# Optimization experiments

Measured on AMD Instinct MI355X. Metric: run time of the kernel, lower is better.

## Reference

```python
import jax, jax.numpy as jnp
import numpy as np

B, S, D = 4, 512, 512


def setup_inputs() -> dict:
    key = jax.random.key(0)
    k0, k1, k2 = jax.random.split(key, 3)
    x = jax.random.normal(k0, (B, S, D), jnp.float32)
    W1 = jax.random.normal(k1, (D, D // 2), jnp.float32) / np.sqrt(D).astype(np.float32)
    b1 = jnp.zeros((D // 2,), jnp.float32)
    W2 = jax.random.normal(k2, (D // 2, 1), jnp.float32) / np.sqrt(D // 2).astype(np.float32)
    b2 = jnp.zeros((1,), jnp.float32)
    # deterministic ragged durations in the module's ~10-30 frame range
    durations = jnp.broadcast_to(8 + (jnp.arange(S, dtype=jnp.int32) % 32), (B, S))
    total_length = int(np.asarray(durations).sum())  # 48128, static
    return dict(x=x, W1=W1, b1=b1, W2=W2, b2=b2, durations=durations,
                total_length=total_length)


def reference(x, W1, b1, W2, b2, durations, total_length):
    # --- duration-predictor MLP (Linear -> ReLU -> Linear -> Softplus) ---
    h = jax.nn.relu(jnp.einsum('bsd,df->bsf', x, W1) + b1)
    dur_mlp = jax.nn.softplus(jnp.einsum('bsf,fo->bso', h, W2) + b2)[..., 0]  # [B,S]

    # --- length regulation: gather + linear interpolation ---
    # torch code uses durations of batch row 0 for all batch elements, and
    # allocates total_length = sum over the WHOLE batch (trailing zeros kept).
    dur0 = durations[0].astype(jnp.int32)          # [S]
    csum = jnp.cumsum(dur0)                         # [S], csum[-1] = used length L
    L = csum[-1]
    t = jnp.arange(total_length, dtype=jnp.int32)   # [T]
    tok = jnp.searchsorted(csum, t, side='right')   # token index per output frame
    valid = t < L
    ic = jnp.minimum(tok, S - 1)
    j = t - (csum[ic] - dur0[ic])                   # offset within token's frames
    # last token: pure repeat (alpha=0); others: lerp toward x[:, i+1]
    alpha = jnp.where(ic == S - 1, 0.0,
                      j.astype(x.dtype) / dur0[ic].astype(x.dtype))  # [T]
    left = x[:, ic]                                 # [B,T,D]
    right = x[:, jnp.minimum(ic + 1, S - 1)]        # [B,T,D]
    a = alpha[None, :, None]
    expanded = (1.0 - a) * left + a * right
    expanded = jnp.where(valid[None, :, None], expanded, 0.0)
    return expanded, dur_mlp
```

## Files before the change

### kernel.cpp

```cpp
#include <hip/hip_runtime.h>
#include <math.h>

#define Bn 4
#define Sn 512
#define Dn 512
#define Fn 256
#define RROWS 8

struct Ent { float alpha; int ic; };

typedef float v4f __attribute__((ext_vector_type(4)));

__global__ __launch_bounds__(512) void prep_kernel(const int* __restrict__ dur,
                                                   Ent* __restrict__ tab, int T) {
    __shared__ int csum[Sn];
    int tid = threadIdx.x;
    csum[tid] = dur[tid];
    __syncthreads();
    #pragma unroll
    for (int off = 1; off < Sn; off <<= 1) {
        int add = (tid >= off) ? csum[tid - off] : 0;
        __syncthreads();
        csum[tid] += add;
        __syncthreads();
    }
    int L = csum[Sn - 1];
    int t = blockIdx.x * Sn + tid;
    if (t >= T) return;
    Ent e;
    if (t >= L) {
        e.alpha = 0.f; e.ic = -1;
    } else {
        int lo = 0, hi = Sn;
        while (lo < hi) {
            int mid = (lo + hi) >> 1;
            if (csum[mid] <= t) lo = mid + 1; else hi = mid;
        }
        int ic = lo;
        int start = ic ? csum[ic - 1] : 0;
        int d = csum[ic] - start;
        e.ic = ic;
        e.alpha = (ic == Sn - 1) ? 0.f : (float)(t - start) / (float)d;
    }
    tab[t] = e;
}

__global__ __launch_bounds__(256) void mlp_kernel(const float* __restrict__ x,
                                                  const float* __restrict__ W1,
                                                  const float* __restrict__ b1,
                                                  const float* __restrict__ W2,
                                                  const float* __restrict__ b2,
                                                  float* __restrict__ out_dur) {
    __shared__ float xs[RROWS][Dn];
    __shared__ float red[4][RROWS];
    int f = threadIdx.x;
    int r0 = blockIdx.x * RROWS;

    const float4* src = (const float4*)(x + (size_t)r0 * Dn);
    float4* dst = (float4*)(&xs[0][0]);
    for (int i = f; i < RROWS * Dn / 4; i += 256) dst[i] = src[i];
    __syncthreads();

    float acc[RROWS];
    #pragma unroll
    for (int r = 0; r < RROWS; r++) acc[r] = 0.f;

    for (int k = 0; k < Dn; k += 4) {
        float w0 = W1[(k + 0) * Fn + f];
        float w1 = W1[(k + 1) * Fn + f];
        float w2 = W1[(k + 2) * Fn + f];
        float w3 = W1[(k + 3) * Fn + f];
        #pragma unroll
        for (int r = 0; r < RROWS; r++) {
            float4 xv = *(const float4*)&xs[r][k];
            acc[r] += xv.x * w0 + xv.y * w1 + xv.z * w2 + xv.w * w3;
        }
    }

    float bb = b1[f], wf = W2[f];
    float p[RROWS];
    #pragma unroll
    for (int r = 0; r < RROWS; r++) {
        float h = acc[r] + bb;
        h = h > 0.f ? h : 0.f;
        p[r] = h * wf;
    }

    int lane = f & 63, wv = f >> 6;
    #pragma unroll
    for (int r = 0; r < RROWS; r++) {
        float v = p[r];
        #pragma unroll
        for (int off = 32; off > 0; off >>= 1) v += __shfl_down(v, off, 64);
        if (lane == 0) red[wv][r] = v;
    }
    __syncthreads();
    if (f < RROWS) {
        float z = red[0][f] + red[1][f] + red[2][f] + red[3][f] + b2[0];
        float sp = fmaxf(z, 0.f) + log1pf(expf(-fabsf(z)));
        out_dur[r0 + f] = sp;
    }
}

__global__ __launch_bounds__(256) void expand_kernel(const float* __restrict__ x,
                                                     const Ent* __restrict__ tab,
                                                     float* __restrict__ out, int T) {
    int idx = blockIdx.x * 256 + threadIdx.x;
    int total = T << 7;
    if (idx >= total) return;
    int b = blockIdx.y;
    int t = idx >> 7;
    int d4 = idx & 127;

    Ent e = tab[t];
    float4 res;
    if (e.ic < 0) {
        res = make_float4(0.f, 0.f, 0.f, 0.f);
    } else {
        const float* xb = x + (size_t)b * (Sn * Dn);
        int icr = e.ic + 1; if (icr > Sn - 1) icr = Sn - 1;
        float4 l = ((const float4*)(xb + (size_t)e.ic * Dn))[d4];
        float4 r = ((const float4*)(xb + (size_t)icr * Dn))[d4];
        float a = e.alpha, na = 1.f - a;
        res.x = na * l.x + a * r.x;
        res.y = na * l.y + a * r.y;
        res.z = na * l.z + a * r.z;
        res.w = na * l.w + a * r.w;
    }
    float4* op = (float4*)(out + ((size_t)b * T + t) * Dn) + d4;
    __builtin_nontemporal_store(*(const v4f*)&res, (v4f*)op);
}

extern "C" void kernel_launch(void* const* d_in, const int* in_sizes, int n_in,
                              void* d_out, int out_size, void* d_ws, size_t ws_size,
                              hipStream_t stream) {
    const float* x   = (const float*)d_in[0];
    const float* W1  = (const float*)d_in[1];
    const float* b1  = (const float*)d_in[2];
    const float* W2  = (const float*)d_in[3];
    const float* b2  = (const float*)d_in[4];
    const int* durs  = (const int*)d_in[5];
    float* out = (float*)d_out;

    int T = (out_size - Bn * Sn) / (Bn * Dn);
    Ent* tab = (Ent*)d_ws;

    dim3 pgrid((T + Sn - 1) / Sn);
    prep_kernel<<<pgrid, Sn, 0, stream>>>(durs, tab, T);

    float* dur_out = out + ((size_t)out_size - Bn * Sn);
    mlp_kernel<<<dim3((Bn * Sn) / RROWS), 256, 0, stream>>>(x, W1, b1, W2, b2, dur_out);

    int total4 = T * (Dn / 4);
    dim3 egrid((total4 + 255) / 256, Bn);
    expand_kernel<<<egrid, 256, 0, stream>>>(x, tab, out, T);
}
```

Baseline: 427.6 us.

## Merge prep and MLP kernels into one launch; give expand one wavefront per frame

```diff
diff --git a/kernel.cpp b/kernel.cpp
--- a/kernel.cpp
+++ b/kernel.cpp
@@ -11,124 +11,126 @@
 
 typedef float v4f __attribute__((ext_vector_type(4)));
 
-__global__ __launch_bounds__(512) void prep_kernel(const int* __restrict__ dur,
-                                                   Ent* __restrict__ tab, int T) {
-    __shared__ int csum[Sn];
+#define PREP_BLKS (48128 / 256)
+#define MLP_BLKS  ((Bn * Sn) / RROWS)
+
+__global__ __launch_bounds__(256) void prep_mlp_kernel(
+        const int* __restrict__ dur, Ent* __restrict__ tab, int T,
+        const float* __restrict__ x,  const float* __restrict__ W1,
+        const float* __restrict__ b1, const float* __restrict__ W2,
+        const float* __restrict__ b2, float* __restrict__ out_dur) {
     int tid = threadIdx.x;
-    csum[tid] = dur[tid];
-    __syncthreads();
-    #pragma unroll
-    for (int off = 1; off < Sn; off <<= 1) {
-        int add = (tid >= off) ? csum[tid - off] : 0;
+
+    if (blockIdx.x < PREP_BLKS) {
+        __shared__ int cs[Sn];
+        cs[tid]       = dur[tid];
+        cs[tid + 256] = dur[tid + 256];
         __syncthreads();
-        csum[tid] += add;
+        #pragma unroll
+        for (int off = 1; off < Sn; off <<= 1) {
+            int a0 = (tid >= off) ? cs[tid - off] : 0;
+            int p1 = tid + 256;
+            int a1 = (p1 >= off) ? cs[p1 - off] : 0;
+            __syncthreads();
+            cs[tid] += a0; cs[p1] += a1;
+            __syncthreads();
+        }
+        int L = cs[Sn - 1];
+        int t = blockIdx.x * 256 + tid;
+        if (t >= T) return;
+        Ent e;
+        if (t >= L) {
+            e.alpha = 0.f; e.ic = -1;
+        } else {
+            int lo = 0, hi = Sn;
+            while (lo < hi) {
+                int mid = (lo + hi) >> 1;
+                if (cs[mid] <= t) lo = mid + 1; else hi = mid;
+            }
+            int ic = lo;
+            int start = ic ? cs[ic - 1] : 0;
+            int d = cs[ic] - start;
+            e.ic = ic;
+            e.alpha = (ic == Sn - 1) ? 0.f : (float)(t - start) / (float)d;
+        }
+        tab[t] = e;
+    } else {
+        __shared__ float xs[RROWS][Dn];
+        __shared__ float red[4][RROWS];
+        int f = tid;
+        int r0 = (blockIdx.x - PREP_BLKS) * RROWS;
+
+        const float4* src = (const float4*)(x + (size_t)r0 * Dn);
+        float4* dst = (float4*)(&xs[0][0]);
+        for (int i = f; i < RROWS * Dn / 4; i += 256) dst[i] = src[i];
         __syncthreads();
-    }
-    int L = csum[Sn - 1];
-    int t = blockIdx.x * Sn + tid;
-    if (t >= T) return;
-    Ent e;
-    if (t >= L) {
-        e.alpha = 0.f; e.ic = -1;
-    } else {
-        int lo = 0, hi = Sn;
-        while (lo < hi) {
-            int mid = (lo + hi) >> 1;
-            if (csum[mid] <= t) lo = mid + 1; else hi = mid;
+
+        float acc[RROWS];
+        #pragma unroll
+        for (int r = 0; r < RROWS; r++) acc[r] = 0.f;
+
+        for (int k = 0; k < Dn; k += 4) {
+            float w0 = W1[(k + 0) * Fn + f];
+            float w1 = W1[(k + 1) * Fn + f];
+            float w2 = W1[(k + 2) * Fn + f];
+            float w3 = W1[(k + 3) * Fn + f];
+            #pragma unroll
+            for (int r = 0; r < RROWS; r++) {
+                float4 xv = *(const float4*)&xs[r][k];
+                acc[r] += xv.x * w0 + xv.y * w1 + xv.z * w2 + xv.w * w3;
+            }
         }
-        int ic = lo;
-        int start = ic ? csum[ic - 1] : 0;
-        int d = csum[ic] - start;
-        e.ic = ic;
-        e.alpha = (ic == Sn - 1) ? 0.f : (float)(t - start) / (float)d;
-    }
-    tab[t] = e;
-}
 
-__global__ __launch_bounds__(256) void mlp_kernel(const float* __restrict__ x,
-                                                  const float* __restrict__ W1,
-                                                  const float* __restrict__ b1,
-                                                  const float* __restrict__ W2,
-                                                  const float* __restrict__ b2,
-                                                  float* __restrict__ out_dur) {
-    __shared__ float xs[RROWS][Dn];
-    __shared__ float red[4][RROWS];
-    int f = threadIdx.x;
-    int r0 = blockIdx.x * RROWS;
-
-    const float4* src = (const float4*)(x + (size_t)r0 * Dn);
-    float4* dst = (float4*)(&xs[0][0]);
-    for (int i = f; i < RROWS * Dn / 4; i += 256) dst[i] = src[i];
-    __syncthreads();
-
-    float acc[RROWS];
-    #pragma unroll
-    for (int r = 0; r < RROWS; r++) acc[r] = 0.f;
-
-    for (int k = 0; k < Dn; k += 4) {
-        float w0 = W1[(k + 0) * Fn + f];
-        float w1 = W1[(k + 1) * Fn + f];
-        float w2 = W1[(k + 2) * Fn + f];
-        float w3 = W1[(k + 3) * Fn + f];
+        float bb = b1[f], wf = W2[f];
+        int lane = f & 63, wv = f >> 6;
         #pragma unroll
         for (int r = 0; r < RROWS; r++) {
-            float4 xv = *(const float4*)&xs[r][k];
-            acc[r] += xv.x * w0 + xv.y * w1 + xv.z * w2 + xv.w * w3;
+            float h = acc[r] + bb;
+            h = h > 0.f ? h : 0.f;
+            float v = h * wf;
+            #pragma unroll
+            for (int off = 32; off > 0; off >>= 1) v += __shfl_down(v, off, 64);
+            if (lane == 0) red[wv][r] = v;
         }
-    }
-
-    float bb = b1[f], wf = W2[f];
-    float p[RROWS];
-    #pragma unroll
-    for (int r = 0; r < RROWS; r++) {
-        float h = acc[r] + bb;
-        h = h > 0.f ? h : 0.f;
-        p[r] = h * wf;
-    }
-
-    int lane = f & 63, wv = f >> 6;
-    #pragma unroll
-    for (int r = 0; r < RROWS; r++) {
-        float v = p[r];
-        #pragma unroll
-        for (int off = 32; off > 0; off >>= 1) v += __shfl_down(v, off, 64);
-        if (lane == 0) red[wv][r] = v;
-    }
-    __syncthreads();
-    if (f < RROWS) {
-        float z = red[0][f] + red[1][f] + red[2][f] + red[3][f] + b2[0];
-        float sp = fmaxf(z, 0.f) + log1pf(expf(-fabsf(z)));
-        out_dur[r0 + f] = sp;
+        __syncthreads();
+        if (f < RROWS) {
+            float z = red[0][f] + red[1][f] + red[2][f] + red[3][f] + b2[0];
+            float sp = fmaxf(z, 0.f) + log1pf(expf(-fabsf(z)));
+            out_dur[r0 + f] = sp;
+        }
     }
 }
 
 __global__ __launch_bounds__(256) void expand_kernel(const float* __restrict__ x,
                                                      const Ent* __restrict__ tab,
                                                      float* __restrict__ out, int T) {
-    int idx = blockIdx.x * 256 + threadIdx.x;
-    int total = T << 7;
-    if (idx >= total) return;
+    int lane = threadIdx.x & 63;
+    int r = threadIdx.x >> 6;
+    int t = blockIdx.x * 4 + r;
     int b = blockIdx.y;
-    int t = idx >> 7;
-    int d4 = idx & 127;
 
     Ent e = tab[t];
-    float4 res;
+    float* orow = out + ((size_t)b * T + t) * Dn;
+
     if (e.ic < 0) {
-        res = make_float4(0.f, 0.f, 0.f, 0.f);
+        v4f z = {0.f, 0.f, 0.f, 0.f};
+        __builtin_nontemporal_store(z, (v4f*)orow + lane);
+        __builtin_nontemporal_store(z, (v4f*)orow + lane + 64);
     } else {
         const float* xb = x + (size_t)b * (Sn * Dn);
         int icr = e.ic + 1; if (icr > Sn - 1) icr = Sn - 1;
-        float4 l = ((const float4*)(xb + (size_t)e.ic * Dn))[d4];
-        float4 r = ((const float4*)(xb + (size_t)icr * Dn))[d4];
+        const float4* lp = (const float4*)(xb + (size_t)e.ic * Dn);
+        const float4* rp = (const float4*)(xb + (size_t)icr * Dn);
         float a = e.alpha, na = 1.f - a;
-        res.x = na * l.x + a * r.x;
-        res.y = na * l.y + a * r.y;
-        res.z = na * l.z + a * r.z;
-        res.w = na * l.w + a * r.w;
+        float4 l0 = lp[lane],      r0 = rp[lane];
+        float4 l1 = lp[lane + 64], r1 = rp[lane + 64];
+        v4f o0 = {na * l0.x + a * r0.x, na * l0.y + a * r0.y,
+                  na * l0.z + a * r0.z, na * l0.w + a * r0.w};
+        v4f o1 = {na * l1.x + a * r1.x, na * l1.y + a * r1.y,
+                  na * l1.z + a * r1.z, na * l1.w + a * r1.w};
+        __builtin_nontemporal_store(o0, (v4f*)orow + lane);
+        __builtin_nontemporal_store(o1, (v4f*)orow + lane + 64);
     }
-    float4* op = (float4*)(out + ((size_t)b * T + t) * Dn) + d4;
-    __builtin_nontemporal_store(*(const v4f*)&res, (v4f*)op);
 }
 
 extern "C" void kernel_launch(void* const* d_in, const int* in_sizes, int n_in,
@@ -145,13 +147,10 @@
     int T = (out_size - Bn * Sn) / (Bn * Dn);
     Ent* tab = (Ent*)d_ws;
 
-    dim3 pgrid((T + Sn - 1) / Sn);
-    prep_kernel<<<pgrid, Sn, 0, stream>>>(durs, tab, T);
+    float* dur_out = out + ((size_t)out_size - Bn * Sn);
+    prep_mlp_kernel<<<dim3(PREP_BLKS + MLP_BLKS), 256, 0, stream>>>(
+        durs, tab, T, x, W1, b1, W2, b2, dur_out);
 
-    float* dur_out = out + ((size_t)out_size - Bn * Sn);
-    mlp_kernel<<<dim3((Bn * Sn) / RROWS), 256, 0, stream>>>(x, W1, b1, W2, b2, dur_out);
-
-    int total4 = T * (Dn / 4);
-    dim3 egrid((total4 + 255) / 256, Bn);
+    dim3 egrid(T / 4, Bn);
     expand_kernel<<<egrid, 256, 0, stream>>>(x, tab, out, T);
 }
```

Result: no change. 435.5 us (+1.9%).
